# Optimization experiments

Hardware: AMD Instinct MI355X
Metric: run time of the kernel (lower is better)

The kernel has to match this reference:

```python
import jax, jax.numpy as jnp
import numpy as np

NUM_HEADS = 16
HEAD_DIM = 128
ROPE_BASE = 10000.0


def _rotate_half(x):
    x1, x2 = jnp.split(x, 2, axis=-1)
    return jnp.concatenate([-x2, x1], axis=-1)


def setup_inputs() -> dict:
    key = jax.random.key(0)
    ks = jax.random.split(key, 6)
    B, S, H = 2, 2048, 2048
    hidden_states = jax.random.normal(ks[0], (B, S, H), dtype=jnp.float32)
    # causal additive mask: 0 on/below diagonal, large negative above
    causal = jnp.tril(jnp.ones((S, S), dtype=bool))
    attention_mask = jnp.where(causal, 0.0, -1e9).astype(jnp.float32)[None, None]
    position_ids = jnp.broadcast_to(jnp.arange(S, dtype=jnp.int64), (B, S))
    sc = 1.0 / np.sqrt(H)
    Wq = jax.random.normal(ks[1], (H, H), dtype=jnp.float32) * sc
    Wk = jax.random.normal(ks[2], (H, H), dtype=jnp.float32) * sc
    Wv = jax.random.normal(ks[3], (H, H), dtype=jnp.float32) * sc
    Wo = jax.random.normal(ks[4], (H, H), dtype=jnp.float32) * sc
    return {"hidden_states": hidden_states, "attention_mask": attention_mask,
            "position_ids": position_ids, "Wq": Wq, "Wk": Wk, "Wv": Wv, "Wo": Wo}


def reference(hidden_states, attention_mask, position_ids, Wq, Wk, Wv, Wo):
    B, S, H = hidden_states.shape
    nH, hd = NUM_HEADS, HEAD_DIM
    # projections (torch Linear: x @ W.T)
    q = (hidden_states @ Wq.T).reshape(B, S, nH, hd).transpose(0, 2, 1, 3)  # [B,nH,S,hd]
    k = (hidden_states @ Wk.T).reshape(B, S, nH, hd).transpose(0, 2, 1, 3)
    v = (hidden_states @ Wv.T).reshape(B, S, nH, hd).transpose(0, 2, 1, 3)
    # rotary embeddings: cos/sin cache over positions, duplicated to full head_dim
    inv_freq = 1.0 / (ROPE_BASE ** (jnp.arange(0, hd, 2, dtype=jnp.float32) / hd))  # [hd/2]
    t = jnp.arange(S, dtype=jnp.float32)
    freqs = jnp.outer(t, inv_freq)                       # [S, hd/2]
    emb = jnp.concatenate([freqs, freqs], axis=-1)       # [S, hd]
    cos = jnp.cos(emb)[position_ids][:, None]            # [B,1,S,hd]
    sin = jnp.sin(emb)[position_ids][:, None]
    q = q * cos + _rotate_half(q) * sin
    k = k * cos + _rotate_half(k) * sin
    # eager attention
    scores = jnp.einsum('bhqd,bhkd->bhqk', q, k) / np.sqrt(hd).astype(np.float32)
    scores = scores + attention_mask
    attn = jax.nn.softmax(scores, axis=-1)
    out = jnp.einsum('bhqk,bhkd->bhqd', attn, v)         # [B,nH,S,hd]
    out = out.transpose(0, 2, 1, 3).reshape(B, S, H)
    return out @ Wo.T
```

## Files before the change

### kernel.cpp

```cpp
#include <hip/hip_runtime.h>
#include <cstdint>
#include <cstddef>

#define NH    16
#define HD    128
#define SEQ   2048
#define HID   2048
#define BATCH 2
#define MTOT  (BATCH*SEQ)

#define SCALE 0.08838834764831845f
#define L2E   1.4426950408889634f
#define KSCL  (0.08838834764831845f * 1.4426950408889634f)
#define L2_10K_D64 0.20762050593046458f

typedef __bf16 bf16x8 __attribute__((ext_vector_type(8)));
typedef float  floatx4 __attribute__((ext_vector_type(4)));

__device__ __forceinline__ unsigned short f2bf(float f) {
  union { float f; unsigned u; } v; v.f = f;
  unsigned u = v.u;
  return (unsigned short)((u + 0x7FFFu + ((u >> 16) & 1u)) >> 16);
}
__device__ __forceinline__ float bf2f(unsigned short h) {
  union { unsigned u; float f; } v; v.u = ((unsigned)h) << 16; return v.f;
}

__device__ __forceinline__ void gld16(const unsigned short* g, unsigned short* l) {
  auto gp = reinterpret_cast<const __attribute__((address_space(1))) void*>(
      reinterpret_cast<uintptr_t>(g));
  auto lp = reinterpret_cast<__attribute__((address_space(3))) void*>(
      reinterpret_cast<uintptr_t>(l));
  __builtin_amdgcn_global_load_lds(gp, lp, 16, 0, 0);
}

__global__ void cvt_all(const float* __restrict__ X,
                        const float* __restrict__ Wq, const float* __restrict__ Wk,
                        const float* __restrict__ Wv, const float* __restrict__ Wo,
                        unsigned short* __restrict__ Xb,
                        unsigned short* __restrict__ Wqb, unsigned short* __restrict__ Wkb,
                        unsigned short* __restrict__ Wvb, unsigned short* __restrict__ Wob) {
  int i = blockIdx.x * blockDim.x + threadIdx.x;
  const float* src; unsigned short* dst; int k;
  if (i < (1 << 21)) { src = X; dst = Xb; k = i; }
  else {
    int j = i - (1 << 21);
    int seg = j >> 20; k = j & ((1 << 20) - 1);
    src = (seg == 0) ? Wq : (seg == 1) ? Wk : (seg == 2) ? Wv : Wo;
    dst = (seg == 0) ? Wqb : (seg == 1) ? Wkb : (seg == 2) ? Wvb : Wob;
  }
  float4 v = reinterpret_cast<const float4*>(src)[k];
  ushort4 o;
  o.x = f2bf(v.x); o.y = f2bf(v.y); o.z = f2bf(v.z); o.w = f2bf(v.w);
  reinterpret_cast<ushort4*>(dst)[k] = o;
}

__global__ void rope_qk(unsigned short* __restrict__ Q,
                        unsigned short* __restrict__ Kk) {
  int idx = blockIdx.x * blockDim.x + threadIdx.x;
  if (idx >= BATCH * NH * SEQ * 64) return;
  int i  = idx & 63;
  int s  = (idx >> 6) & (SEQ - 1);
  int bh = idx >> 17;
  float freq = exp2f(-(float)i * L2_10K_D64);
  float th = (float)s * freq;
  float cx = cosf(th), sy = sinf(th);
  size_t base = ((size_t)bh * SEQ + s) * HD;
  float qa = bf2f(Q[base + i]), qb = bf2f(Q[base + i + 64]);
  Q[base + i]      = f2bf(qa * cx - qb * sy);
  Q[base + i + 64] = f2bf(qb * cx + qa * sy);
  float ka = bf2f(Kk[base + i]), kb = bf2f(Kk[base + i + 64]);
  Kk[base + i]      = f2bf(ka * cx - kb * sy);
  Kk[base + i + 64] = f2bf(kb * cx + ka * sy);
}

__device__ __forceinline__ void gemm_core(const unsigned short* __restrict__ A,
                                          const unsigned short* __restrict__ B,
                                          int K, int mBase, int nBase,
                                          unsigned short* As, unsigned short* Bs,
                                          floatx4 acc[4][4]) {
  int tid  = threadIdx.x;
  int wave = tid >> 6, lane = tid & 63;
  int l16  = lane & 15, quad = lane >> 4;
  int wm   = wave >> 1, wn = wave & 1;

  const unsigned short* Ag = A + (size_t)mBase * K;
  const unsigned short* Bg = B + (size_t)nBase * K;

  for (int k0 = 0; k0 < K; k0 += 32) {
    __syncthreads();
#pragma unroll
    for (int r = 0; r < 2; ++r) {
      int row0 = wave * 32 + r * 16;
      int grow = row0 + (lane >> 2);
      int gcol = k0 + (lane & 3) * 8;
      gld16(Ag + (size_t)grow * K + gcol, As + row0 * 32 + lane * 8);
      gld16(Bg + (size_t)grow * K + gcol, Bs + row0 * 32 + lane * 8);
    }
    __syncthreads();

    bf16x8 af[4], bfr[4];
#pragma unroll
    for (int t = 0; t < 4; ++t) {
      af[t]  = *reinterpret_cast<const bf16x8*>(&As[(wm * 64 + t * 16 + l16) * 32 + quad * 8]);
      bfr[t] = *reinterpret_cast<const bf16x8*>(&Bs[(wn * 64 + t * 16 + l16) * 32 + quad * 8]);
    }
#pragma unroll
    for (int tm = 0; tm < 4; ++tm)
#pragma unroll
      for (int tn = 0; tn < 4; ++tn)
        acc[tm][tn] = __builtin_amdgcn_mfma_f32_16x16x32_bf16(af[tm], bfr[tn], acc[tm][tn], 0, 0, 0);
  }
}

__global__ __launch_bounds__(256)
void gemm_qkv(const unsigned short* __restrict__ Xb,
              const unsigned short* __restrict__ Wq,
              const unsigned short* __restrict__ Wk,
              const unsigned short* __restrict__ Wv,
              unsigned short* __restrict__ Qo,
              unsigned short* __restrict__ Ko,
              unsigned short* __restrict__ Vto) {
  __shared__ unsigned short As[128 * 32];
  __shared__ unsigned short Bs[128 * 32];
  int z = blockIdx.z;
  const unsigned short* W = (z == 0) ? Wq : (z == 1) ? Wk : Wv;
  int mBase = blockIdx.y * 128, nBase = blockIdx.x * 128;

  floatx4 acc[4][4];
#pragma unroll
  for (int i = 0; i < 4; ++i)
#pragma unroll
    for (int j = 0; j < 4; ++j) acc[i][j] = {0.f, 0.f, 0.f, 0.f};

  gemm_core(Xb, W, HID, mBase, nBase, As, Bs, acc);

  int tid = threadIdx.x;
  int wave = tid >> 6, lane = tid & 63;
  int l16 = lane & 15, quad = lane >> 4;
  int wm = wave >> 1, wn = wave & 1;

#pragma unroll
  for (int tm = 0; tm < 4; ++tm) {
    int mrow = mBase + wm * 64 + tm * 16 + quad * 4;
#pragma unroll
    for (int tn = 0; tn < 4; ++tn) {
      int n = nBase + wn * 64 + tn * 16 + l16;
      int hh = n >> 7, d = n & 127;
      if (z < 2) {
        unsigned short* dst = (z == 0) ? Qo : Ko;
#pragma unroll
        for (int r = 0; r < 4; ++r) {
          int m = mrow + r;
          int bb = m >> 11, s = m & (SEQ - 1);
          dst[(((size_t)bb * NH + hh) * SEQ + s) * HD + d] = f2bf(acc[tm][tn][r]);
        }
      } else {
        int bb = mrow >> 11, s = mrow & (SEQ - 1);
        ushort4 pk;
        pk.x = f2bf(acc[tm][tn][0]); pk.y = f2bf(acc[tm][tn][1]);
        pk.z = f2bf(acc[tm][tn][2]); pk.w = f2bf(acc[tm][tn][3]);
        *reinterpret_cast<ushort4*>(&Vto[(((size_t)bb * NH + hh) * HD + d) * SEQ + s]) = pk;
      }
    }
  }
}

__global__ __launch_bounds__(256)
void gemm_out(const unsigned short* __restrict__ Ob,
              const unsigned short* __restrict__ Wo,
              float* __restrict__ out) {
  __shared__ unsigned short As[128 * 32];
  __shared__ unsigned short Bs[128 * 32];
  int mBase = blockIdx.y * 128, nBase = blockIdx.x * 128;

  floatx4 acc[4][4];
#pragma unroll
  for (int i = 0; i < 4; ++i)
#pragma unroll
    for (int j = 0; j < 4; ++j) acc[i][j] = {0.f, 0.f, 0.f, 0.f};

  gemm_core(Ob, Wo, HID, mBase, nBase, As, Bs, acc);

  int tid = threadIdx.x;
  int wave = tid >> 6, lane = tid & 63;
  int l16 = lane & 15, quad = lane >> 4;
  int wm = wave >> 1, wn = wave & 1;

#pragma unroll
  for (int tm = 0; tm < 4; ++tm) {
    int mrow = mBase + wm * 64 + tm * 16 + quad * 4;
#pragma unroll
    for (int tn = 0; tn < 4; ++tn) {
      int n = nBase + wn * 64 + tn * 16 + l16;
#pragma unroll
      for (int r = 0; r < 4; ++r)
        out[(size_t)(mrow + r) * HID + n] = acc[tm][tn][r];
    }
  }
}

__global__ __launch_bounds__(512)
void attn_kernel(const unsigned short* __restrict__ Q,
                 const unsigned short* __restrict__ K,
                 const unsigned short* __restrict__ Vt,
                 unsigned short* __restrict__ Ob) {
  __shared__ unsigned short Ks[32 * 136];
  __shared__ unsigned short Vs[128 * 40];
  __shared__ unsigned short Ps[8][16 * 40];

  int qt = 15 - blockIdx.y;
  int bh = blockIdx.x;
  int b = bh >> 4, h = bh & 15;
  int q0 = qt * 128;
  int tid = threadIdx.x;
  int wave = tid >> 6, lane = tid & 63;
  int l16 = lane & 15, quad = lane >> 4;

  const size_t headQ = (size_t)bh * SEQ * HD;
  const size_t headV = (size_t)bh * HD * SEQ;

  bf16x8 qf[4];
  {
    int qrow = q0 + wave * 16 + l16;
    const unsigned short* qp = Q + headQ + (size_t)qrow * HD + quad * 8;
#pragma unroll
    for (int c = 0; c < 4; ++c)
      qf[c] = *reinterpret_cast<const bf16x8*>(qp + c * 32);
  }

  floatx4 oacc[8];
#pragma unroll
  for (int i = 0; i < 8; ++i) oacc[i] = {0.f, 0.f, 0.f, 0.f};
  float rs[4];
#pragma unroll
  for (int r = 0; r < 4; ++r) rs[r] = 0.f;

  int qq = q0 + wave * 16 + quad * 4;
  int qmax = q0 + wave * 16 + 15;
  unsigned short* pw = Ps[wave];

  int nkt = q0 / 32 + 4;
  for (int kt = 0; kt < nkt; ++kt) {
    int k0 = kt * 32;
    __syncthreads();
    {
      int row = tid >> 4, dc = (tid & 15) * 8;
      *reinterpret_cast<uint4*>(&Ks[row * 136 + dc]) =
        *reinterpret_cast<const uint4*>(&K[headQ + (size_t)(k0 + row) * HD + dc]);
    }
    {
      int row = tid >> 2, kc = (tid & 3) * 8;
      *reinterpret_cast<uint4*>(&Vs[row * 40 + kc]) =
        *reinterpret_cast<const uint4*>(&Vt[headV + (size_t)row * SEQ + k0 + kc]);
    }
    __syncthreads();

    if (k0 <= qmax) {
      floatx4 sc[2];
#pragma unroll
      for (int nt = 0; nt < 2; ++nt) {
        floatx4 s4 = {0.f, 0.f, 0.f, 0.f};
#pragma unroll
        for (int c = 0; c < 4; ++c) {
          bf16x8 kf = *reinterpret_cast<const bf16x8*>(&Ks[(nt * 16 + l16) * 136 + c * 32 + quad * 8]);
          s4 = __builtin_amdgcn_mfma_f32_16x16x32_bf16(qf[c], kf, s4, 0, 0, 0);
        }
        sc[nt] = s4;
      }

#pragma unroll
      for (int nt = 0; nt < 2; ++nt) {
        int kk = k0 + nt * 16 + l16;
#pragma unroll
        for (int r = 0; r < 4; ++r) {
          float arg = (kk <= qq + r) ? fmaf(sc[nt][r], KSCL, -32.0f) : -1e9f;
          float p = exp2f(arg);
          rs[r] += p;
          pw[(quad * 4 + r) * 40 + nt * 16 + l16] = f2bf(p);
        }
      }
      __asm__ __volatile__("s_waitcnt lgkmcnt(0)" ::: "memory");
      bf16x8 pf = *reinterpret_cast<const bf16x8*>(&pw[l16 * 40 + quad * 8]);

#pragma unroll
      for (int dt = 0; dt < 8; ++dt) {
        bf16x8 vf = *reinterpret_cast<const bf16x8*>(&Vs[(dt * 16 + l16) * 40 + quad * 8]);
        oacc[dt] = __builtin_amdgcn_mfma_f32_16x16x32_bf16(pf, vf, oacc[dt], 0, 0, 0);
      }
    }
  }

#pragma unroll
  for (int off = 1; off < 16; off <<= 1)
#pragma unroll
    for (int r = 0; r < 4; ++r) rs[r] += __shfl_xor(rs[r], off, 16);

  float inv[4];
#pragma unroll
  for (int r = 0; r < 4; ++r) inv[r] = 1.0f / rs[r];
#pragma unroll
  for (int dt = 0; dt < 8; ++dt)
#pragma unroll
    for (int r = 0; r < 4; ++r) {
      int s = q0 + wave * 16 + quad * 4 + r;
      Ob[(((size_t)b * SEQ + s) * NH + h) * HD + dt * 16 + l16] = f2bf(oacc[dt][r] * inv[r]);
    }
}

extern "C" void kernel_launch(void* const* d_in, const int* in_sizes, int n_in,
                              void* d_out, int out_size, void* d_ws, size_t ws_size,
                              hipStream_t stream) {
  const float* X  = (const float*)d_in[0];
  const float* Wq = (const float*)d_in[3];
  const float* Wk = (const float*)d_in[4];
  const float* Wv = (const float*)d_in[5];
  const float* Wo = (const float*)d_in[6];

  char* w = (char*)d_ws;
  size_t off = 0;
  auto alloc = [&](size_t bytes) { char* p = w + off; off += (bytes + 255) & ~(size_t)255; return p; };

  unsigned short* Xb  = (unsigned short*)alloc((size_t)MTOT * HID * 2);
  unsigned short* Wqb = (unsigned short*)alloc((size_t)HID * HID * 2);
  unsigned short* Wkb = (unsigned short*)alloc((size_t)HID * HID * 2);
  unsigned short* Wvb = (unsigned short*)alloc((size_t)HID * HID * 2);
  unsigned short* Wob = (unsigned short*)alloc((size_t)HID * HID * 2);
  unsigned short* Qb  = (unsigned short*)alloc((size_t)BATCH * NH * SEQ * HD * 2);
  unsigned short* Kb  = (unsigned short*)alloc((size_t)BATCH * NH * SEQ * HD * 2);
  unsigned short* Vtb = (unsigned short*)alloc((size_t)BATCH * NH * HD * SEQ * 2);
  unsigned short* Obf = (unsigned short*)alloc((size_t)BATCH * SEQ * NH * HD * 2);

  const int nAll4 = (MTOT * HID + 4 * HID * HID) / 4;
  cvt_all<<<nAll4 / 256, 256, 0, stream>>>(X, Wq, Wk, Wv, Wo, Xb, Wqb, Wkb, Wvb, Wob);

  gemm_qkv<<<dim3(HID / 128, MTOT / 128, 3), 256, 0, stream>>>(Xb, Wqb, Wkb, Wvb, Qb, Kb, Vtb);

  rope_qk<<<(BATCH * NH * SEQ * 64) / 256, 256, 0, stream>>>(Qb, Kb);

  attn_kernel<<<dim3(BATCH * NH, SEQ / 128), 512, 0, stream>>>(Qb, Kb, Vtb, Obf);

  gemm_out<<<dim3(HID / 128, MTOT / 128), 256, 0, stream>>>(Obf, Wob, (float*)d_out);
}
```

Before: 419.3 us.

## Replace QKV GEMM with 256x256 double-buffered direct-to-LDS pipelined kernel

Replaces the simple 128x128 QKV projection GEMM with a 256x256-tile, 512-thread kernel. It loads global memory straight into LDS (gld16) with XOR-swizzled layout, double-buffers K-tiles of 64, and interleaves the staging loads with MFMA sub-blocks using explicit barriers, waitcnts and s_setprio. This aims to raise MFMA utilisation and data reuse and to hide global-load latency behind compute. In exchange it needs heavy register use and hand-tuned synchronisation, and the larger tiles cut the grid to 384 blocks.

```diff
diff --git a/kernel.cpp b/kernel.cpp
--- a/kernel.cpp
+++ b/kernel.cpp
@@ -74,6 +74,160 @@
   Kk[base + i + 64] = f2bf(kb * cx + ka * sy);
 }
 
+
+#define SBAR      asm volatile("s_barrier" ::: "memory")
+#define WAITLGKM  asm volatile("s_waitcnt lgkmcnt(0)" ::: "memory")
+#define WAITVM(n) asm volatile("s_waitcnt vmcnt(" #n ")" ::: "memory")
+#define PRIO1     __builtin_amdgcn_s_setprio(1)
+#define PRIO0     __builtin_amdgcn_s_setprio(0)
+
+#define STAGE(gptr, sptr, buf, half, t8)                                        \
+  {                                                                             \
+    _Pragma("unroll")                                                           \
+    for (int j_ = 0; j_ < 2; ++j_) {                                            \
+      int G_   = j_ * 512 + tid;                                                \
+      int row_ = G_ >> 3;                                                       \
+      int cgs_ = (G_ & 7) ^ (row_ & 7);                                         \
+      gld16(gptr + (size_t)((half) * 128 + row_) * HID + (t8) * 64 + cgs_ * 8,  \
+            sptr + (buf) * 16384 + (half) * 8192 + G_ * 8);                     \
+    }                                                                           \
+  }
+
+#define LDA(buf, qm)                                                            \
+  _Pragma("unroll")                                                             \
+  for (int mr_ = 0; mr_ < 4; ++mr_)                                             \
+    _Pragma("unroll")                                                           \
+    for (int ks_ = 0; ks_ < 2; ++ks_)                                           \
+      af[mr_][ks_] = *reinterpret_cast<const bf16x8*>(                          \
+          &As[(buf) * 16384 + (wm * 128 + (qm) * 64 + mr_ * 16 + l16) * 64 + cgo[ks_]]);
+
+#define LDB2(buf, nr0)                                                          \
+  _Pragma("unroll")                                                             \
+  for (int nr_ = 0; nr_ < 2; ++nr_)                                             \
+    _Pragma("unroll")                                                           \
+    for (int ks_ = 0; ks_ < 2; ++ks_)                                           \
+      bfr[(nr0) + nr_][ks_] = *reinterpret_cast<const bf16x8*>(                 \
+          &Bs[(buf) * 16384 + (wn * 64 + ((nr0) + nr_) * 16 + l16) * 64 + cgo[ks_]]);
+
+#define MM(qm, qn)                                                              \
+  _Pragma("unroll")                                                             \
+  for (int ks_ = 0; ks_ < 2; ++ks_)                                             \
+    _Pragma("unroll")                                                           \
+    for (int mr_ = 0; mr_ < 4; ++mr_)                                           \
+      _Pragma("unroll")                                                         \
+      for (int nr_ = 0; nr_ < 2; ++nr_)                                         \
+        acc[(qm) * 4 + mr_][(qn) * 2 + nr_] =                                   \
+            __builtin_amdgcn_mfma_f32_16x16x32_bf16(                            \
+                af[mr_][ks_], bfr[(qn) * 2 + nr_][ks_],                         \
+                acc[(qm) * 4 + mr_][(qn) * 2 + nr_], 0, 0, 0);
+
+__global__ __launch_bounds__(512)
+void gemm_qkv256(const unsigned short* __restrict__ Xb,
+                 const unsigned short* __restrict__ Wq,
+                 const unsigned short* __restrict__ Wk,
+                 const unsigned short* __restrict__ Wv,
+                 unsigned short* __restrict__ Qo,
+                 unsigned short* __restrict__ Ko,
+                 unsigned short* __restrict__ Vto) {
+  __shared__ unsigned short As[2 * 16384];
+  __shared__ unsigned short Bs[2 * 16384];
+
+  const int z = blockIdx.z;
+  const unsigned short* W = (z == 0) ? Wq : (z == 1) ? Wk : Wv;
+  const int mBase = blockIdx.y * 256, nBase = blockIdx.x * 256;
+  const unsigned short* Ag = Xb + (size_t)mBase * HID;
+  const unsigned short* Bg = W  + (size_t)nBase * HID;
+
+  const int tid  = threadIdx.x;
+  const int wave = tid >> 6, lane = tid & 63;
+  const int l16  = lane & 15, quad = lane >> 4;
+  const int wm   = wave >> 2, wn = wave & 3;
+  const int xr   = l16 & 7;
+  const int cgo[2] = { ((quad) ^ xr) * 8, ((quad + 4) ^ xr) * 8 };
+
+  floatx4 acc[8][4];
+#pragma unroll
+  for (int i = 0; i < 8; ++i)
+#pragma unroll
+    for (int j = 0; j < 4; ++j) acc[i][j] = {0.f, 0.f, 0.f, 0.f};
+
+  bf16x8 af[4][2], bfr[4][2];
+
+  STAGE(Bg, Bs, 0, 0, 0); STAGE(Bg, Bs, 0, 1, 0);
+  STAGE(Ag, As, 0, 0, 0); STAGE(Ag, As, 0, 1, 0);
+  STAGE(Bg, Bs, 1, 0, 1); STAGE(Bg, Bs, 1, 1, 1);
+  WAITVM(4);
+  SBAR;
+
+#pragma unroll 1
+  for (int i = 0; i < 15; ++i) {
+    const int t = 2 * i;
+    LDA(0, 0); LDB2(0, 0);
+    STAGE(Ag, As, 1, 0, t + 1);
+    SBAR; WAITLGKM; PRIO1; MM(0, 0); PRIO0; SBAR;
+    LDB2(0, 2);
+    STAGE(Ag, As, 1, 1, t + 1);
+    SBAR; WAITLGKM; PRIO1; MM(0, 1); PRIO0; SBAR;
+    LDA(0, 1);
+    STAGE(Bg, Bs, 0, 0, t + 2);
+    SBAR; WAITLGKM; PRIO1; MM(1, 0); PRIO0; SBAR;
+    STAGE(Bg, Bs, 0, 1, t + 2);
+    SBAR; PRIO1; MM(1, 1); PRIO0; WAITVM(4); SBAR;
+    LDA(1, 0); LDB2(1, 0);
+    STAGE(Ag, As, 0, 0, t + 2);
+    SBAR; WAITLGKM; PRIO1; MM(0, 0); PRIO0; SBAR;
+    LDB2(1, 2);
+    STAGE(Ag, As, 0, 1, t + 2);
+    SBAR; WAITLGKM; PRIO1; MM(0, 1); PRIO0; SBAR;
+    LDA(1, 1);
+    STAGE(Bg, Bs, 1, 0, t + 3);
+    SBAR; WAITLGKM; PRIO1; MM(1, 0); PRIO0; SBAR;
+    STAGE(Bg, Bs, 1, 1, t + 3);
+    SBAR; PRIO1; MM(1, 1); PRIO0; WAITVM(4); SBAR;
+  }
+
+  LDA(0, 0); LDB2(0, 0);
+  STAGE(Ag, As, 1, 0, 31);
+  SBAR; WAITLGKM; PRIO1; MM(0, 0); PRIO0; SBAR;
+  LDB2(0, 2);
+  STAGE(Ag, As, 1, 1, 31);
+  SBAR; WAITLGKM; PRIO1; MM(0, 1); PRIO0; SBAR;
+  LDA(0, 1);
+  SBAR; WAITLGKM; PRIO1; MM(1, 0); PRIO0; SBAR;
+  SBAR; PRIO1; MM(1, 1); PRIO0; WAITVM(0); SBAR;
+  LDA(1, 0); LDB2(1, 0);
+  SBAR; WAITLGKM; PRIO1; MM(0, 0); PRIO0; SBAR;
+  LDB2(1, 2);
+  SBAR; WAITLGKM; PRIO1; MM(0, 1); PRIO0; SBAR;
+  LDA(1, 1);
+  SBAR; WAITLGKM; PRIO1; MM(1, 0); MM(1, 1); PRIO0;
+
+#pragma unroll
+  for (int mr = 0; mr < 8; ++mr) {
+    int mrow = mBase + wm * 128 + mr * 16 + quad * 4;
+#pragma unroll
+    for (int nr = 0; nr < 4; ++nr) {
+      int n = nBase + wn * 64 + nr * 16 + l16;
+      int hh = n >> 7, d = n & 127;
+      if (z < 2) {
+        unsigned short* dst = (z == 0) ? Qo : Ko;
+#pragma unroll
+        for (int r = 0; r < 4; ++r) {
+          int m = mrow + r;
+          int bb = m >> 11, s = m & (SEQ - 1);
+          dst[(((size_t)bb * NH + hh) * SEQ + s) * HD + d] = f2bf(acc[mr][nr][r]);
+        }
+      } else {
+        int bb = mrow >> 11, s = mrow & (SEQ - 1);
+        ushort4 pk;
+        pk.x = f2bf(acc[mr][nr][0]); pk.y = f2bf(acc[mr][nr][1]);
+        pk.z = f2bf(acc[mr][nr][2]); pk.w = f2bf(acc[mr][nr][3]);
+        *reinterpret_cast<ushort4*>(&Vto[(((size_t)bb * NH + hh) * HD + d) * SEQ + s]) = pk;
+      }
+    }
+  }
+}
+
 __device__ __forceinline__ void gemm_core(const unsigned short* __restrict__ A,
                                           const unsigned short* __restrict__ B,
                                           int K, int mBase, int nBase,
@@ -114,59 +268,6 @@
 }
 
 __global__ __launch_bounds__(256)
-void gemm_qkv(const unsigned short* __restrict__ Xb,
-              const unsigned short* __restrict__ Wq,
-              const unsigned short* __restrict__ Wk,
-              const unsigned short* __restrict__ Wv,
-              unsigned short* __restrict__ Qo,
-              unsigned short* __restrict__ Ko,
-              unsigned short* __restrict__ Vto) {
-  __shared__ unsigned short As[128 * 32];
-  __shared__ unsigned short Bs[128 * 32];
-  int z = blockIdx.z;
-  const unsigned short* W = (z == 0) ? Wq : (z == 1) ? Wk : Wv;
-  int mBase = blockIdx.y * 128, nBase = blockIdx.x * 128;
-
-  floatx4 acc[4][4];
-#pragma unroll
-  for (int i = 0; i < 4; ++i)
-#pragma unroll
-    for (int j = 0; j < 4; ++j) acc[i][j] = {0.f, 0.f, 0.f, 0.f};
-
-  gemm_core(Xb, W, HID, mBase, nBase, As, Bs, acc);
-
-  int tid = threadIdx.x;
-  int wave = tid >> 6, lane = tid & 63;
-  int l16 = lane & 15, quad = lane >> 4;
-  int wm = wave >> 1, wn = wave & 1;
-
-#pragma unroll
-  for (int tm = 0; tm < 4; ++tm) {
-    int mrow = mBase + wm * 64 + tm * 16 + quad * 4;
-#pragma unroll
-    for (int tn = 0; tn < 4; ++tn) {
-      int n = nBase + wn * 64 + tn * 16 + l16;
-      int hh = n >> 7, d = n & 127;
-      if (z < 2) {
-        unsigned short* dst = (z == 0) ? Qo : Ko;
-#pragma unroll
-        for (int r = 0; r < 4; ++r) {
-          int m = mrow + r;
-          int bb = m >> 11, s = m & (SEQ - 1);
-          dst[(((size_t)bb * NH + hh) * SEQ + s) * HD + d] = f2bf(acc[tm][tn][r]);
-        }
-      } else {
-        int bb = mrow >> 11, s = mrow & (SEQ - 1);
-        ushort4 pk;
-        pk.x = f2bf(acc[tm][tn][0]); pk.y = f2bf(acc[tm][tn][1]);
-        pk.z = f2bf(acc[tm][tn][2]); pk.w = f2bf(acc[tm][tn][3]);
-        *reinterpret_cast<ushort4*>(&Vto[(((size_t)bb * NH + hh) * HD + d) * SEQ + s]) = pk;
-      }
-    }
-  }
-}
-
-__global__ __launch_bounds__(256)
 void gemm_out(const unsigned short* __restrict__ Ob,
               const unsigned short* __restrict__ Wo,
               float* __restrict__ out) {
@@ -334,7 +435,7 @@
   const int nAll4 = (MTOT * HID + 4 * HID * HID) / 4;
   cvt_all<<<nAll4 / 256, 256, 0, stream>>>(X, Wq, Wk, Wv, Wo, Xb, Wqb, Wkb, Wvb, Wob);
 
-  gemm_qkv<<<dim3(HID / 128, MTOT / 128, 3), 256, 0, stream>>>(Xb, Wqb, Wkb, Wvb, Qb, Kb, Vtb);
+  gemm_qkv256<<<dim3(HID / 256, MTOT / 256, 3), 512, 0, stream>>>(Xb, Wqb, Wkb, Wvb, Qb, Kb, Vtb);
 
   rope_qk<<<(BATCH * NH * SEQ * 64) / 256, 256, 0, stream>>>(Qb, Kb);
 
```

Result: faster. 409.1 us (-2.4%).
